# Kernel tuning notes

Hardware: AMD Instinct MI355X
Metric: run time of the kernel (lower is better)

## Reference

```python
import jax, jax.numpy as jnp
from jax import lax
import numpy as np

B, T, C = 16, 2048, 1024
H, K = 16, 31
R = C // H
P = K - 1  # padding_l (causal)


def setup_inputs() -> dict:
    key = jax.random.key(0)
    kx, kw = jax.random.split(key)
    x = jax.random.normal(kx, (B, T, C), dtype=jnp.float32)
    # kaiming_uniform_(a=sqrt(5)) on (H, 1, K): fan_in = K, bound = 1/sqrt(K)
    bound = 1.0 / np.sqrt(K)
    weight = jax.random.uniform(kw, (H, 1, K), dtype=jnp.float32,
                                minval=-bound, maxval=bound)
    return {"x": x, "weight": weight}


def reference(x, weight):
    # weight_softmax=True: softmax over kernel dim (done in fp32, as in source)
    w = jax.nn.softmax(weight.reshape(H, K).astype(jnp.float32), axis=-1)
    w = w.astype(x.dtype)
    # Each head's kernel is shared across R = C//H channels -> depthwise kernel (C, 1, K)
    w_c = jnp.repeat(w, R, axis=0)            # (C, K)
    kernel = w_c[:, None, :]                  # (C, 1, K) in OIH layout
    x_t = jnp.transpose(x, (0, 2, 1))         # (B, C, T)
    # Cross-correlation with left pad P, right pad K-1-P (same math as the
    # banded-matrix _forward_expanded path / unfold1d + matmul)
    out = lax.conv_general_dilated(
        x_t, kernel,
        window_strides=(1,),
        padding=[(P, K - 1 - P)],
        feature_group_count=C,
        dimension_numbers=("NCH", "OIH", "NCH"),
    )                                         # (B, C, T)
    return jnp.transpose(out, (0, 2, 1))      # (B, T, C)
```

## Files before the change

### kernel.cpp

```cpp
#include <hip/hip_runtime.h>
#include <math.h>

#define TPB  256
#define KW   31
#define HALO 30
#define TT   8
#define BT   128
#define RQ   40
constexpr int B_ = 16, T_ = 2048, C_ = 1024, H_ = 16;
constexpr int C4  = C_ / 4;
constexpr int QPH = 16;

typedef float f32x4 __attribute__((ext_vector_type(4)));

__device__ inline float rfl(float v) {
    return __builtin_bit_cast(float, __builtin_amdgcn_readfirstlane(__builtin_bit_cast(int, v)));
}

__global__ __launch_bounds__(TPB) void lconv_kernel(const float* __restrict__ x,
                                                    const float* __restrict__ w,
                                                    float* __restrict__ out) {
    __shared__ float smem[RQ * 256];
    const int h   = blockIdx.x;
    const int b   = blockIdx.z;
    const int t0b = blockIdx.y * BT;
    const int tid  = threadIdx.x;
    const int lane = tid & 63, wid = tid >> 6;
    const int qrow = lane >> 4, chunk = lane & 15;

    const float* xh = x + (size_t)b * T_ * C_ + h * 64;
    #pragma unroll
    for (int q = wid; q < RQ; q += 4) {
        const int t = t0b - HALO + 4 * q + qrow;
        if (t >= 0) {
            const float* src = xh + (size_t)((t < T_ - 1) ? t : T_ - 1) * C_ + chunk * 4;
            __builtin_amdgcn_global_load_lds(
                (const __attribute__((address_space(1))) uint32_t*)src,
                (__attribute__((address_space(3))) uint32_t*)(smem + q * 256),
                16, 0, 0);
        }
    }

    float wv[KW];
    {
        float v[KW]; float m = -1e30f;
        #pragma unroll
        for (int k = 0; k < KW; ++k) { v[k] = w[h * KW + k]; m = fmaxf(m, v[k]); }
        float s = 0.f;
        #pragma unroll
        for (int k = 0; k < KW; ++k) { v[k] = __expf(v[k] - m); s += v[k]; }
        const float inv = 1.f / s;
        #pragma unroll
        for (int j = 0; j < KW; ++j) wv[j] = rfl(v[KW - 1 - j] * inv);
    }

    if (blockIdx.y == 0) {
        for (int k = tid; k < HALO * 64; k += TPB) smem[k] = 0.f;
    }
    __syncthreads();

    const int quad = tid & 15;
    const int sub  = tid >> 4;

    f32x4 acc[TT];
    #pragma unroll
    for (int i = 0; i < TT; ++i) acc[i] = (f32x4)0.f;

    const f32x4* sm4 = (const f32x4*)smem;
    #pragma unroll
    for (int sr = 0; sr < TT + HALO; ++sr) {
        const f32x4 v = sm4[(sub * TT + sr) * QPH + quad];
        const int ilo = (sr - HALO < 0) ? 0 : sr - HALO;
        const int ihi = (sr < TT - 1) ? sr : TT - 1;
        #pragma unroll
        for (int i = ilo; i <= ihi; ++i) {
            acc[i] += wv[i + HALO - sr] * v;
        }
    }

    f32x4* po = (f32x4*)out + ((size_t)b * T_ + t0b + sub * TT) * C4 + h * QPH + quad;
    #pragma unroll
    for (int i = 0; i < TT; ++i)
        __builtin_nontemporal_store(acc[i], po + (size_t)i * C4);
}

extern "C" void kernel_launch(void* const* d_in, const int* in_sizes, int n_in,
                              void* d_out, int out_size, void* d_ws, size_t ws_size,
                              hipStream_t stream) {
    const float* x = (const float*)d_in[0];
    const float* w = (const float*)d_in[1];
    float* out = (float*)d_out;

    dim3 grid(H_, T_ / BT, B_);
    hipLaunchKernelGGL(lconv_kernel, grid, dim3(TPB), 0, stream, x, w, out);
}
```

Before: 46.70 us.

## Shrink blocks to single wavefront and replace barrier with waitcnt

Each block becomes one 64-thread wavefront that handles 32 time rows and stages 64 rows (32 of them halo) into LDS. Because only one wave touches the shared tile, __syncthreads is replaced by an explicit s_waitcnt plus a scheduling barrier. The aim is to drop cross-wave barrier cost and raise block count for better scheduling. The trade-off is that halo reloads rise from about 30/128 to 32/32 rows per tile, doubling global reads.

```diff
diff --git a/kernel.cpp b/kernel.cpp
--- a/kernel.cpp
+++ b/kernel.cpp
@@ -1,15 +1,14 @@
 #include <hip/hip_runtime.h>
 #include <math.h>
 
-#define TPB  256
-#define KW   31
-#define HALO 30
-#define TT   8
-#define BT   128
-#define RQ   40
+#define TPB   64
+#define KW    31
+#define HALO  30
+#define TT    8
+#define WROWS 32
+#define SROWS 64
 constexpr int B_ = 16, T_ = 2048, C_ = 1024, H_ = 16;
-constexpr int C4  = C_ / 4;
-constexpr int QPH = 16;
+constexpr int C4 = C_ / 4;
 
 typedef float f32x4 __attribute__((ext_vector_type(4)));
 
@@ -20,20 +19,21 @@
 __global__ __launch_bounds__(TPB) void lconv_kernel(const float* __restrict__ x,
                                                     const float* __restrict__ w,
                                                     float* __restrict__ out) {
-    __shared__ float smem[RQ * 256];
-    const int h   = blockIdx.x;
-    const int b   = blockIdx.z;
-    const int t0b = blockIdx.y * BT;
-    const int tid  = threadIdx.x;
-    const int lane = tid & 63, wid = tid >> 6;
+    __shared__ float smem[SROWS * 64];
+    const int h    = blockIdx.x;
+    const int y    = blockIdx.y;
+    const int b    = blockIdx.z;
+    const int t0   = y * WROWS;
+    const int lane = threadIdx.x;
     const int qrow = lane >> 4, chunk = lane & 15;
+    const int quad = lane & 15, sl = lane >> 2 >> 2;
 
     const float* xh = x + (size_t)b * T_ * C_ + h * 64;
     #pragma unroll
-    for (int q = wid; q < RQ; q += 4) {
-        const int t = t0b - HALO + 4 * q + qrow;
-        if (t >= 0) {
-            const float* src = xh + (size_t)((t < T_ - 1) ? t : T_ - 1) * C_ + chunk * 4;
+    for (int q = 0; q < 16; ++q) {
+        const int tq = t0 - 32 + 4 * q;
+        if (tq >= 0) {
+            const float* src = xh + (size_t)(tq + qrow) * C_ + chunk * 4;
             __builtin_amdgcn_global_load_lds(
                 (const __attribute__((address_space(1))) uint32_t*)src,
                 (__attribute__((address_space(3))) uint32_t*)(smem + q * 256),
@@ -54,13 +54,14 @@
         for (int j = 0; j < KW; ++j) wv[j] = rfl(v[KW - 1 - j] * inv);
     }
 
-    if (blockIdx.y == 0) {
-        for (int k = tid; k < HALO * 64; k += TPB) smem[k] = 0.f;
+    if (y == 0) {
+        f32x4* s4 = (f32x4*)smem;
+        #pragma unroll
+        for (int k = 0; k < 8; ++k) s4[k * 64 + lane] = (f32x4)0.f;
     }
-    __syncthreads();
 
-    const int quad = tid & 15;
-    const int sub  = tid >> 4;
+    asm volatile("s_waitcnt vmcnt(0) lgkmcnt(0)" ::: "memory");
+    __builtin_amdgcn_sched_barrier(0);
 
     f32x4 acc[TT];
     #pragma unroll
@@ -69,7 +70,7 @@
     const f32x4* sm4 = (const f32x4*)smem;
     #pragma unroll
     for (int sr = 0; sr < TT + HALO; ++sr) {
-        const f32x4 v = sm4[(sub * TT + sr) * QPH + quad];
+        const f32x4 v = sm4[(8 * sl + 2 + sr) * 16 + quad];
         const int ilo = (sr - HALO < 0) ? 0 : sr - HALO;
         const int ihi = (sr < TT - 1) ? sr : TT - 1;
         #pragma unroll
@@ -78,7 +79,7 @@
         }
     }
 
-    f32x4* po = (f32x4*)out + ((size_t)b * T_ + t0b + sub * TT) * C4 + h * QPH + quad;
+    f32x4* po = (f32x4*)out + ((size_t)b * T_ + t0 + 8 * sl) * C4 + h * 16 + quad;
     #pragma unroll
     for (int i = 0; i < TT; ++i)
         __builtin_nontemporal_store(acc[i], po + (size_t)i * C4);
@@ -91,6 +92,6 @@
     const float* w = (const float*)d_in[1];
     float* out = (float*)d_out;
 
-    dim3 grid(H_, T_ / BT, B_);
+    dim3 grid(H_, T_ / WROWS, B_);
     hipLaunchKernelGGL(lconv_kernel, grid, dim3(TPB), 0, stream, x, w, out);
 }
```

After: 46.65 us. Within noise of the previous version (-0.1%).
